# Kernel optimization log

Measured on AMD Instinct MI355X. Metric: run time of the kernel, lower is better.

Reference implementation:

```python
import jax, jax.numpy as jnp
import numpy as np

BN_EPS = 1e-5  # torch BatchNorm1d default


def setup_inputs() -> dict:
    key = jax.random.key(0)
    k = jax.random.split(key, 5)
    B, D, L = 4096, 4096, 4  # batch, width, num layers (3 hidden + 1 output)
    x = jax.random.normal(k[0], (B, D), dtype=jnp.float32)
    # Per-layer Linear weights stored as [L, in, out]; scaled like xavier-ish init.
    W = jax.random.normal(k[1], (L, D, D), dtype=jnp.float32) * (1.0 / np.sqrt(D))
    b = jax.random.normal(k[2], (L, D), dtype=jnp.float32) * 0.01
    gamma = jax.random.uniform(k[3], (L, D), dtype=jnp.float32, minval=0.5, maxval=1.5)
    beta = jax.random.normal(k[4], (L, D), dtype=jnp.float32) * 0.1
    return {"x": x, "W": W, "b": b, "gamma": gamma, "beta": beta}


def _layer(h, W_l, b_l, gamma_l, beta_l):
    # one big GEMM replaces the per-neuron GEMV loop + stack
    h = h @ W_l + b_l  # [B, out]
    # BatchNorm1d, training mode: biased batch stats over the batch dim
    mu = jnp.mean(h, axis=0)
    var = jnp.var(h, axis=0)
    h = (h - mu) * jax.lax.rsqrt(var + BN_EPS) * gamma_l + beta_l
    return jax.nn.relu(h)


def reference(x, W, b, gamma, beta):
    out = x
    for l in range(W.shape[0]):  # small fixed layer count
        out = _layer(out, W[l], b[l], gamma[l], beta[l])
    # nn.Softmax(dim=0): softmax over the batch dimension, as in the original
    return jax.nn.softmax(out, axis=0)
```

## Files before the change

### kernel.cpp

```cpp
#include <hip/hip_runtime.h>
#include <stdint.h>

#define DIMD 4096
#define DIMB 4096
#define NLAYER 4
#define NT (DIMD / 64)

typedef unsigned short u16;
typedef __attribute__((ext_vector_type(4))) float f32x4;
typedef __attribute__((ext_vector_type(8))) __bf16 bf16x8;

__device__ __forceinline__ u16 f2bf(float f) {
    union { float f; uint32_t u; } v; v.f = f;
    return (u16)((v.u + 0x7fffu + ((v.u >> 16) & 1u)) >> 16);
}
__device__ __forceinline__ float bf2f(u16 u) {
    union { uint32_t u; float f; } v; v.u = ((uint32_t)u) << 16;
    return v.f;
}

__global__ void k_cvt(const float* __restrict__ in, u16* __restrict__ out) {
    int i = (blockIdx.x * 256 + threadIdx.x) * 4;
    float4 v = *reinterpret_cast<const float4*>(in + i);
    ushort4 r;
    r.x = f2bf(v.x); r.y = f2bf(v.y); r.z = f2bf(v.z); r.w = f2bf(v.w);
    *reinterpret_cast<ushort4*>(out + i) = r;
}

__global__ void k_trans(const float* __restrict__ W, u16* __restrict__ Wt) {
    __shared__ float tile[64][65];
    const int t = threadIdx.x;
    const size_t loff = (size_t)blockIdx.z * DIMD * DIMD;
    const int n0 = blockIdx.x * 64, k0 = blockIdx.y * 64;
    const int kr = t >> 4, c4 = (t & 15) * 4;
    #pragma unroll
    for (int r = 0; r < 4; ++r) {
        float4 v = *reinterpret_cast<const float4*>(W + loff + (size_t)(k0 + kr + r * 16) * DIMD + n0 + c4);
        tile[kr + r * 16][c4 + 0] = v.x;
        tile[kr + r * 16][c4 + 1] = v.y;
        tile[kr + r * 16][c4 + 2] = v.z;
        tile[kr + r * 16][c4 + 3] = v.w;
    }
    __syncthreads();
    const int nr = t >> 4, k4 = (t & 15) * 4;
    #pragma unroll
    for (int r = 0; r < 4; ++r) {
        int n = nr + r * 16;
        ushort4 o;
        o.x = f2bf(tile[k4 + 0][n]);
        o.y = f2bf(tile[k4 + 1][n]);
        o.z = f2bf(tile[k4 + 2][n]);
        o.w = f2bf(tile[k4 + 3][n]);
        *reinterpret_cast<ushort4*>(Wt + loff + (size_t)(n0 + n) * DIMD + k0 + k4) = o;
    }
}

#define GLD(g, l) __builtin_amdgcn_global_load_lds( \
    (__attribute__((address_space(1))) void*)(g),   \
    (__attribute__((address_space(3))) void*)(l), 16, 0, 0)

__global__ __launch_bounds__(512, 2) void k_gemm(
        const u16* __restrict__ A, const u16* __restrict__ Bt,
        const float* __restrict__ bias, u16* __restrict__ H,
        float* __restrict__ csum, float* __restrict__ csum2) {
    __shared__ __attribute__((aligned(16))) u16 As[2 * 256 * 64];
    __shared__ __attribute__((aligned(16))) u16 Bs[2 * 256 * 64];
    const int tid = threadIdx.x;
    const int lane = tid & 63, wv = tid >> 6;
    const int wm = wv >> 2, wn = wv & 3;
    const int bid = blockIdx.y * 16 + blockIdx.x;
    const int swz = (bid & 7) * 32 + (bid >> 3);
    const int bm = swz >> 4, bn = swz & 15;
    const int lr = lane & 15, lk = lane >> 4;

    const int r0 = tid >> 3;
    const int cswz = (tid & 7) ^ (r0 & 7);
    const u16* gA = A  + (size_t)(bm * 256 + r0) * DIMD + cswz * 8;
    const u16* gB = Bt + (size_t)(bn * 256 + r0) * DIMD + cswz * 8;

#define STAGE_A(h, t, buf) do { \
    const u16* _s = gA + (size_t)(h) * 128 * DIMD + (size_t)(t) * 64; \
    u16* _d = As + (buf) * 16384 + (h) * 8192 + wv * 512; \
    GLD(_s, _d); GLD(_s + (size_t)64 * DIMD, _d + 4096); \
} while (0)
#define STAGE_B(h, t, buf) do { \
    const u16* _s = gB + (size_t)(h) * 128 * DIMD + (size_t)(t) * 64; \
    u16* _d = Bs + (buf) * 16384 + (h) * 8192 + wv * 512; \
    GLD(_s, _d); GLD(_s + (size_t)64 * DIMD, _d + 4096); \
} while (0)

    int aoff[4][2], boff[2][2];
    #pragma unroll
    for (int mf = 0; mf < 4; ++mf)
        #pragma unroll
        for (int ks = 0; ks < 2; ++ks) {
            int row = wm * 128 + mf * 16 + lr;
            aoff[mf][ks] = row * 64 + ((ks * 4 + lk) ^ (row & 7)) * 8;
        }
    #pragma unroll
    for (int nf = 0; nf < 2; ++nf)
        #pragma unroll
        for (int ks = 0; ks < 2; ++ks) {
            int row = wn * 64 + nf * 16 + lr;
            boff[nf][ks] = row * 64 + ((ks * 4 + lk) ^ (row & 7)) * 8;
        }

    f32x4 acc[8][4] = {};
    bf16x8 a[4][2], b0[2][2], b1[2][2];

    STAGE_B(0, 0, 0); STAGE_B(1, 0, 0); STAGE_A(0, 0, 0); STAGE_A(1, 0, 0);
    STAGE_B(0, 1, 1); STAGE_B(1, 1, 1); STAGE_A(0, 1, 1); STAGE_A(1, 1, 1);
    asm volatile("s_waitcnt vmcnt(8)" ::: "memory");
    __builtin_amdgcn_s_barrier();

    for (int t = 0; t < NT; ++t) {
        const int cur = t & 1;
        const u16* Ab = As + cur * 16384;
        const u16* Bb = Bs + cur * 16384;
        const bool pf = (t + 2 < NT);

        #pragma unroll
        for (int mf = 0; mf < 4; ++mf)
            #pragma unroll
            for (int ks = 0; ks < 2; ++ks)
                a[mf][ks] = *reinterpret_cast<const bf16x8*>(Ab + aoff[mf][ks]);
        #pragma unroll
        for (int nf = 0; nf < 2; ++nf)
            #pragma unroll
            for (int ks = 0; ks < 2; ++ks)
                b0[nf][ks] = *reinterpret_cast<const bf16x8*>(Bb + boff[nf][ks]);
        __builtin_amdgcn_s_barrier();
        asm volatile("s_waitcnt lgkmcnt(0)" ::: "memory");
        __builtin_amdgcn_s_setprio(1);
        #pragma unroll
        for (int mf = 0; mf < 4; ++mf)
            #pragma unroll
            for (int nf = 0; nf < 2; ++nf)
                #pragma unroll
                for (int ks = 0; ks < 2; ++ks)
                    acc[mf][nf] = __builtin_amdgcn_mfma_f32_16x16x32_bf16(
                        a[mf][ks], b0[nf][ks], acc[mf][nf], 0, 0, 0);
        __builtin_amdgcn_s_setprio(0);
        __builtin_amdgcn_s_barrier();

        #pragma unroll
        for (int nf = 0; nf < 2; ++nf)
            #pragma unroll
            for (int ks = 0; ks < 2; ++ks)
                b1[nf][ks] = *reinterpret_cast<const bf16x8*>(Bb + 2048 + boff[nf][ks]);
        __builtin_amdgcn_s_barrier();
        asm volatile("s_waitcnt lgkmcnt(0)" ::: "memory");
        __builtin_amdgcn_s_setprio(1);
        #pragma unroll
        for (int mf = 0; mf < 4; ++mf)
            #pragma unroll
            for (int nf = 0; nf < 2; ++nf)
                #pragma unroll
                for (int ks = 0; ks < 2; ++ks)
                    acc[mf][2 + nf] = __builtin_amdgcn_mfma_f32_16x16x32_bf16(
                        a[mf][ks], b1[nf][ks], acc[mf][2 + nf], 0, 0, 0);
        __builtin_amdgcn_s_setprio(0);
        __builtin_amdgcn_s_barrier();

        #pragma unroll
        for (int mf = 0; mf < 4; ++mf)
            #pragma unroll
            for (int ks = 0; ks < 2; ++ks)
                a[mf][ks] = *reinterpret_cast<const bf16x8*>(Ab + 4096 + aoff[mf][ks]);
        if (pf) { STAGE_B(0, t + 2, cur); STAGE_B(1, t + 2, cur); }
        __builtin_amdgcn_s_barrier();
        asm volatile("s_waitcnt lgkmcnt(0)" ::: "memory");
        __builtin_amdgcn_s_setprio(1);
        #pragma unroll
        for (int mf = 0; mf < 4; ++mf)
            #pragma unroll
            for (int nf = 0; nf < 2; ++nf)
                #pragma unroll
                for (int ks = 0; ks < 2; ++ks)
                    acc[4 + mf][2 + nf] = __builtin_amdgcn_mfma_f32_16x16x32_bf16(
                        a[mf][ks], b1[nf][ks], acc[4 + mf][2 + nf], 0, 0, 0);
        __builtin_amdgcn_s_setprio(0);
        __builtin_amdgcn_s_barrier();

        if (pf) { STAGE_A(0, t + 2, cur); STAGE_A(1, t + 2, cur); }
        __builtin_amdgcn_s_setprio(1);
        #pragma unroll
        for (int mf = 0; mf < 4; ++mf)
            #pragma unroll
            for (int nf = 0; nf < 2; ++nf)
                #pragma unroll
                for (int ks = 0; ks < 2; ++ks)
                    acc[4 + mf][nf] = __builtin_amdgcn_mfma_f32_16x16x32_bf16(
                        a[mf][ks], b0[nf][ks], acc[4 + mf][nf], 0, 0, 0);
        __builtin_amdgcn_s_setprio(0);
        if (pf) asm volatile("s_waitcnt vmcnt(8)" ::: "memory");
        else    asm volatile("s_waitcnt vmcnt(0)" ::: "memory");
        __builtin_amdgcn_s_barrier();
    }

    #pragma unroll
    for (int nh = 0; nh < 2; ++nh)
        #pragma unroll
        for (int nf = 0; nf < 2; ++nf) {
            int n = nh * 2 + nf;
            int col = bn * 256 + wn * 64 + nh * 32 + nf * 16 + lr;
            float bv = bias[col];
            float s1 = 0.f, s2 = 0.f;
            #pragma unroll
            for (int m = 0; m < 8; ++m) {
                int rbase = bm * 256 + wm * 128 + (m >> 2) * 64 + (m & 3) * 16 + lk * 4;
                #pragma unroll
                for (int r = 0; r < 4; ++r) {
                    float v = acc[m][n][r] + bv;
                    H[(size_t)(rbase + r) * DIMD + col] = f2bf(v);
                    s1 += v; s2 += v * v;
                }
            }
            s1 += __shfl_xor(s1, 16); s1 += __shfl_xor(s1, 32);
            s2 += __shfl_xor(s2, 16); s2 += __shfl_xor(s2, 32);
            if (lk == 0) {
                atomicAdd(&csum[col], s1);
                atomicAdd(&csum2[col], s2);
            }
        }
#undef STAGE_A
#undef STAGE_B
}

__global__ void k_norm(const u16* __restrict__ H, const float* __restrict__ sum,
                       const float* __restrict__ sum2, const float* __restrict__ gamma,
                       const float* __restrict__ beta, u16* __restrict__ o) {
    int j = (blockIdx.x * 256 + threadIdx.x) * 4;
    int i0 = blockIdx.y * 32;
    float4 sm = *reinterpret_cast<const float4*>(sum + j);
    float4 s2 = *reinterpret_cast<const float4*>(sum2 + j);
    float4 gm = *reinterpret_cast<const float4*>(gamma + j);
    float4 bt = *reinterpret_cast<const float4*>(beta + j);
    float s[4], tt[4];
    #pragma unroll
    for (int c = 0; c < 4; ++c) {
        float mu = (&sm.x)[c] * (1.0f / DIMB);
        float var = (&s2.x)[c] * (1.0f / DIMB) - mu * mu;
        s[c] = (&gm.x)[c] * rsqrtf(var + 1e-5f);
        tt[c] = (&bt.x)[c] - mu * s[c];
    }
    for (int i = i0; i < i0 + 32; ++i) {
        ushort4 h = *reinterpret_cast<const ushort4*>(H + (size_t)i * DIMD + j);
        ushort4 r;
        #pragma unroll
        for (int c = 0; c < 4; ++c)
            (&r.x)[c] = f2bf(fmaxf(bf2f((&h.x)[c]) * s[c] + tt[c], 0.0f));
        *reinterpret_cast<ushort4*>(o + (size_t)i * DIMD + j) = r;
    }
}

__global__ void k_esum(const u16* __restrict__ H, const float* __restrict__ sum,
                       const float* __restrict__ sum2, const float* __restrict__ gamma,
                       const float* __restrict__ beta, float* __restrict__ esum) {
    int j = (blockIdx.x * 256 + threadIdx.x) * 4;
    int i0 = blockIdx.y * 32;
    float4 sm = *reinterpret_cast<const float4*>(sum + j);
    float4 s2 = *reinterpret_cast<const float4*>(sum2 + j);
    float4 gm = *reinterpret_cast<const float4*>(gamma + j);
    float4 bt = *reinterpret_cast<const float4*>(beta + j);
    float s[4], tt[4], acc[4] = {0.f, 0.f, 0.f, 0.f};
    #pragma unroll
    for (int c = 0; c < 4; ++c) {
        float mu = (&sm.x)[c] * (1.0f / DIMB);
        float var = (&s2.x)[c] * (1.0f / DIMB) - mu * mu;
        s[c] = (&gm.x)[c] * rsqrtf(var + 1e-5f);
        tt[c] = (&bt.x)[c] - mu * s[c];
    }
    for (int i = i0; i < i0 + 32; ++i) {
        ushort4 h = *reinterpret_cast<const ushort4*>(H + (size_t)i * DIMD + j);
        #pragma unroll
        for (int c = 0; c < 4; ++c)
            acc[c] += __expf(fmaxf(bf2f((&h.x)[c]) * s[c] + tt[c], 0.0f));
    }
    #pragma unroll
    for (int c = 0; c < 4; ++c) atomicAdd(&esum[j + c], acc[c]);
}

__global__ void k_final(const u16* __restrict__ H, const float* __restrict__ sum,
                        const float* __restrict__ sum2, const float* __restrict__ gamma,
                        const float* __restrict__ beta, const float* __restrict__ esum,
                        float* __restrict__ out) {
    int j = (blockIdx.x * 256 + threadIdx.x) * 4;
    int i0 = blockIdx.y * 32;
    float4 sm = *reinterpret_cast<const float4*>(sum + j);
    float4 s2 = *reinterpret_cast<const float4*>(sum2 + j);
    float4 gm = *reinterpret_cast<const float4*>(gamma + j);
    float4 bt = *reinterpret_cast<const float4*>(beta + j);
    float4 es = *reinterpret_cast<const float4*>(esum + j);
    float s[4], tt[4], inv[4];
    #pragma unroll
    for (int c = 0; c < 4; ++c) {
        float mu = (&sm.x)[c] * (1.0f / DIMB);
        float var = (&s2.x)[c] * (1.0f / DIMB) - mu * mu;
        s[c] = (&gm.x)[c] * rsqrtf(var + 1e-5f);
        tt[c] = (&bt.x)[c] - mu * s[c];
        inv[c] = 1.0f / (&es.x)[c];
    }
    for (int i = i0; i < i0 + 32; ++i) {
        ushort4 h = *reinterpret_cast<const ushort4*>(H + (size_t)i * DIMD + j);
        float4 o;
        #pragma unroll
        for (int c = 0; c < 4; ++c)
            (&o.x)[c] = __expf(fmaxf(bf2f((&h.x)[c]) * s[c] + tt[c], 0.0f)) * inv[c];
        *reinterpret_cast<float4*>(out + (size_t)i * DIMD + j) = o;
    }
}

extern "C" void kernel_launch(void* const* d_in, const int* in_sizes, int n_in,
                              void* d_out, int out_size, void* d_ws, size_t ws_size,
                              hipStream_t stream) {
    (void)in_sizes; (void)n_in; (void)out_size; (void)ws_size;
    const float* x     = (const float*)d_in[0];
    const float* W     = (const float*)d_in[1];
    const float* b     = (const float*)d_in[2];
    const float* gamma = (const float*)d_in[3];
    const float* beta  = (const float*)d_in[4];
    float* out = (float*)d_out;

    char* ws = (char*)d_ws;
    u16*  Abf = (u16*)ws;
    u16*  Wt4 = (u16*)(ws + (size_t)32 * 1024 * 1024);
    u16*  Hbf = (u16*)(ws + (size_t)160 * 1024 * 1024);
    float* stats = (float*)(ws + (size_t)192 * 1024 * 1024);
    hipMemsetAsync(stats, 0, (4 * 8192 + 4096) * sizeof(float), stream);

    k_cvt<<<DIMB * DIMD / 1024, 256, 0, stream>>>(x, Abf);
    k_trans<<<dim3(64, 64, 4), 256, 0, stream>>>(W, Wt4);

    for (int l = 0; l < NLAYER; ++l) {
        float* sum = stats + l * 8192;
        float* sum2 = sum + 4096;
        k_gemm<<<dim3(16, 16), 512, 0, stream>>>(Abf, Wt4 + (size_t)l * DIMD * DIMD,
                                                 b + l * DIMD, Hbf, sum, sum2);
        if (l < NLAYER - 1)
            k_norm<<<dim3(4, 128), 256, 0, stream>>>(Hbf, sum, sum2,
                gamma + l * DIMD, beta + l * DIMD, Abf);
        else
            k_esum<<<dim3(4, 128), 256, 0, stream>>>(Hbf, sum, sum2,
                gamma + l * DIMD, beta + l * DIMD, stats + 32768);
    }
    k_final<<<dim3(4, 128), 256, 0, stream>>>(Hbf, stats + 3 * 8192, stats + 3 * 8192 + 4096,
        gamma + 3 * DIMD, beta + 3 * DIMD, stats + 32768, out);
}
```

Baseline: 731.1 us.

## Restructure GEMM main loop into k-step phases and write final layer fp32 into output

Reorders the GEMM inner loop so each phase loads one k-slice of A and B fragments (4x4 MFMA per phase), replaces the A-tile double prefetch with a one-ahead A stage and two-ahead B stage, and uses partial lgkmcnt waits with sched_barriers. It also drops the block-index swizzle in favour of a plain grid mapping. The last layer's GEMM writes fp32 pre-activations directly into the output buffer, and the softmax kernels read and overwrite it in place, removing the bf16 rounding of the final layer. The plain mapping may lower L2 reuse, and the fp32 store doubles write traffic for that layer.

```diff
diff --git a/kernel.cpp b/kernel.cpp
--- a/kernel.cpp
+++ b/kernel.cpp
@@ -62,15 +62,14 @@
 __global__ __launch_bounds__(512, 2) void k_gemm(
         const u16* __restrict__ A, const u16* __restrict__ Bt,
         const float* __restrict__ bias, u16* __restrict__ H,
+        float* __restrict__ Hf,
         float* __restrict__ csum, float* __restrict__ csum2) {
     __shared__ __attribute__((aligned(16))) u16 As[2 * 256 * 64];
     __shared__ __attribute__((aligned(16))) u16 Bs[2 * 256 * 64];
     const int tid = threadIdx.x;
     const int lane = tid & 63, wv = tid >> 6;
     const int wm = wv >> 2, wn = wv & 3;
-    const int bid = blockIdx.y * 16 + blockIdx.x;
-    const int swz = (bid & 7) * 32 + (bid >> 3);
-    const int bm = swz >> 4, bn = swz & 15;
+    const int bm = blockIdx.y, bn = blockIdx.x;
     const int lr = lane & 15, lk = lane >> 4;
 
     const int r0 = tid >> 3;
@@ -89,7 +88,7 @@
     GLD(_s, _d); GLD(_s + (size_t)64 * DIMD, _d + 4096); \
 } while (0)
 
-    int aoff[4][2], boff[2][2];
+    int aoff[4][2], boff[4][2];
     #pragma unroll
     for (int mf = 0; mf < 4; ++mf)
         #pragma unroll
@@ -98,7 +97,7 @@
             aoff[mf][ks] = row * 64 + ((ks * 4 + lk) ^ (row & 7)) * 8;
         }
     #pragma unroll
-    for (int nf = 0; nf < 2; ++nf)
+    for (int nf = 0; nf < 4; ++nf)
         #pragma unroll
         for (int ks = 0; ks < 2; ++ks) {
             int row = wn * 64 + nf * 16 + lr;
@@ -106,123 +105,113 @@
         }
 
     f32x4 acc[8][4] = {};
-    bf16x8 a[4][2], b0[2][2], b1[2][2];
-
-    STAGE_B(0, 0, 0); STAGE_B(1, 0, 0); STAGE_A(0, 0, 0); STAGE_A(1, 0, 0);
-    STAGE_B(0, 1, 1); STAGE_B(1, 1, 1); STAGE_A(0, 1, 1); STAGE_A(1, 1, 1);
-    asm volatile("s_waitcnt vmcnt(8)" ::: "memory");
+    bf16x8 aS0[4], aS1[4], bk0[4], bk1[4];
+
+    STAGE_B(0, 0, 0); STAGE_B(1, 0, 0);
+    STAGE_B(0, 1, 1); STAGE_B(1, 1, 1);
+    STAGE_A(0, 0, 0); STAGE_A(1, 0, 0);
+    asm volatile("s_waitcnt vmcnt(0)" ::: "memory");
     __builtin_amdgcn_s_barrier();
 
     for (int t = 0; t < NT; ++t) {
         const int cur = t & 1;
         const u16* Ab = As + cur * 16384;
         const u16* Bb = Bs + cur * 16384;
-        const bool pf = (t + 2 < NT);
-
-        #pragma unroll
-        for (int mf = 0; mf < 4; ++mf)
-            #pragma unroll
-            for (int ks = 0; ks < 2; ++ks)
-                a[mf][ks] = *reinterpret_cast<const bf16x8*>(Ab + aoff[mf][ks]);
-        #pragma unroll
-        for (int nf = 0; nf < 2; ++nf)
-            #pragma unroll
-            for (int ks = 0; ks < 2; ++ks)
-                b0[nf][ks] = *reinterpret_cast<const bf16x8*>(Bb + boff[nf][ks]);
-        __builtin_amdgcn_s_barrier();
-        asm volatile("s_waitcnt lgkmcnt(0)" ::: "memory");
+
+        if (t + 1 < NT) { STAGE_A(0, t + 1, cur ^ 1); STAGE_A(1, t + 1, cur ^ 1); }
+        #pragma unroll
+        for (int mf = 0; mf < 4; ++mf)
+            aS0[mf] = *reinterpret_cast<const bf16x8*>(Ab + aoff[mf][0]);
+        #pragma unroll
+        for (int nf = 0; nf < 4; ++nf)
+            bk0[nf] = *reinterpret_cast<const bf16x8*>(Bb + boff[nf][0]);
+        #pragma unroll
+        for (int mf = 0; mf < 4; ++mf)
+            aS1[mf] = *reinterpret_cast<const bf16x8*>(Ab + 4096 + aoff[mf][0]);
+        asm volatile("s_waitcnt lgkmcnt(4)" ::: "memory");
+        __builtin_amdgcn_sched_barrier(0);
         __builtin_amdgcn_s_setprio(1);
         #pragma unroll
         for (int mf = 0; mf < 4; ++mf)
             #pragma unroll
-            for (int nf = 0; nf < 2; ++nf)
-                #pragma unroll
-                for (int ks = 0; ks < 2; ++ks)
-                    acc[mf][nf] = __builtin_amdgcn_mfma_f32_16x16x32_bf16(
-                        a[mf][ks], b0[nf][ks], acc[mf][nf], 0, 0, 0);
+            for (int nf = 0; nf < 4; ++nf)
+                acc[mf][nf] = __builtin_amdgcn_mfma_f32_16x16x32_bf16(
+                    aS0[mf], bk0[nf], acc[mf][nf], 0, 0, 0);
         __builtin_amdgcn_s_setprio(0);
         __builtin_amdgcn_s_barrier();
 
         #pragma unroll
-        for (int nf = 0; nf < 2; ++nf)
-            #pragma unroll
-            for (int ks = 0; ks < 2; ++ks)
-                b1[nf][ks] = *reinterpret_cast<const bf16x8*>(Bb + 2048 + boff[nf][ks]);
-        __builtin_amdgcn_s_barrier();
-        asm volatile("s_waitcnt lgkmcnt(0)" ::: "memory");
+        for (int mf = 0; mf < 4; ++mf)
+            aS0[mf] = *reinterpret_cast<const bf16x8*>(Ab + 4096 + aoff[mf][1]);
+        #pragma unroll
+        for (int nf = 0; nf < 4; ++nf)
+            bk1[nf] = *reinterpret_cast<const bf16x8*>(Bb + boff[nf][1]);
+        asm volatile("s_waitcnt lgkmcnt(8)" ::: "memory");
+        __builtin_amdgcn_sched_barrier(0);
         __builtin_amdgcn_s_setprio(1);
         #pragma unroll
         for (int mf = 0; mf < 4; ++mf)
             #pragma unroll
-            for (int nf = 0; nf < 2; ++nf)
-                #pragma unroll
-                for (int ks = 0; ks < 2; ++ks)
-                    acc[mf][2 + nf] = __builtin_amdgcn_mfma_f32_16x16x32_bf16(
-                        a[mf][ks], b1[nf][ks], acc[mf][2 + nf], 0, 0, 0);
+            for (int nf = 0; nf < 4; ++nf)
+                acc[4 + mf][nf] = __builtin_amdgcn_mfma_f32_16x16x32_bf16(
+                    aS1[mf], bk0[nf], acc[4 + mf][nf], 0, 0, 0);
         __builtin_amdgcn_s_setprio(0);
         __builtin_amdgcn_s_barrier();
 
         #pragma unroll
         for (int mf = 0; mf < 4; ++mf)
-            #pragma unroll
-            for (int ks = 0; ks < 2; ++ks)
-                a[mf][ks] = *reinterpret_cast<const bf16x8*>(Ab + 4096 + aoff[mf][ks]);
-        if (pf) { STAGE_B(0, t + 2, cur); STAGE_B(1, t + 2, cur); }
-        __builtin_amdgcn_s_barrier();
-        asm volatile("s_waitcnt lgkmcnt(0)" ::: "memory");
+            aS1[mf] = *reinterpret_cast<const bf16x8*>(Ab + aoff[mf][1]);
+        asm volatile("s_waitcnt lgkmcnt(4)" ::: "memory");
+        __builtin_amdgcn_sched_barrier(0);
         __builtin_amdgcn_s_setprio(1);
         #pragma unroll
         for (int mf = 0; mf < 4; ++mf)
             #pragma unroll
-            for (int nf = 0; nf < 2; ++nf)
-                #pragma unroll
-                for (int ks = 0; ks < 2; ++ks)
-                    acc[4 + mf][2 + nf] = __builtin_amdgcn_mfma_f32_16x16x32_bf16(
-                        a[mf][ks], b1[nf][ks], acc[4 + mf][2 + nf], 0, 0, 0);
+            for (int nf = 0; nf < 4; ++nf)
+                acc[4 + mf][nf] = __builtin_amdgcn_mfma_f32_16x16x32_bf16(
+                    aS0[mf], bk1[nf], acc[4 + mf][nf], 0, 0, 0);
         __builtin_amdgcn_s_setprio(0);
         __builtin_amdgcn_s_barrier();
 
-        if (pf) { STAGE_A(0, t + 2, cur); STAGE_A(1, t + 2, cur); }
+        if (t + 2 < NT) { STAGE_B(0, t + 2, cur); STAGE_B(1, t + 2, cur); }
+        asm volatile("s_waitcnt lgkmcnt(0)" ::: "memory");
+        __builtin_amdgcn_sched_barrier(0);
         __builtin_amdgcn_s_setprio(1);
         #pragma unroll
         for (int mf = 0; mf < 4; ++mf)
             #pragma unroll
-            for (int nf = 0; nf < 2; ++nf)
-                #pragma unroll
-                for (int ks = 0; ks < 2; ++ks)
-                    acc[4 + mf][nf] = __builtin_amdgcn_mfma_f32_16x16x32_bf16(
-                        a[mf][ks], b0[nf][ks], acc[4 + mf][nf], 0, 0, 0);
+            for (int nf = 0; nf < 4; ++nf)
+                acc[mf][nf] = __builtin_amdgcn_mfma_f32_16x16x32_bf16(
+                    aS1[mf], bk1[nf], acc[mf][nf], 0, 0, 0);
         __builtin_amdgcn_s_setprio(0);
-        if (pf) asm volatile("s_waitcnt vmcnt(8)" ::: "memory");
-        else    asm volatile("s_waitcnt vmcnt(0)" ::: "memory");
+        if (t + 2 < NT) asm volatile("s_waitcnt vmcnt(4)" ::: "memory");
+        else            asm volatile("s_waitcnt vmcnt(0)" ::: "memory");
         __builtin_amdgcn_s_barrier();
     }
 
     #pragma unroll
-    for (int nh = 0; nh < 2; ++nh)
-        #pragma unroll
-        for (int nf = 0; nf < 2; ++nf) {
-            int n = nh * 2 + nf;
-            int col = bn * 256 + wn * 64 + nh * 32 + nf * 16 + lr;
-            float bv = bias[col];
-            float s1 = 0.f, s2 = 0.f;
-            #pragma unroll
-            for (int m = 0; m < 8; ++m) {
-                int rbase = bm * 256 + wm * 128 + (m >> 2) * 64 + (m & 3) * 16 + lk * 4;
-                #pragma unroll
-                for (int r = 0; r < 4; ++r) {
-                    float v = acc[m][n][r] + bv;
-                    H[(size_t)(rbase + r) * DIMD + col] = f2bf(v);
-                    s1 += v; s2 += v * v;
-                }
-            }
-            s1 += __shfl_xor(s1, 16); s1 += __shfl_xor(s1, 32);
-            s2 += __shfl_xor(s2, 16); s2 += __shfl_xor(s2, 32);
-            if (lk == 0) {
-                atomicAdd(&csum[col], s1);
-                atomicAdd(&csum2[col], s2);
+    for (int nf = 0; nf < 4; ++nf) {
+        int col = bn * 256 + wn * 64 + nf * 16 + lr;
+        float bv = bias[col];
+        float s1 = 0.f, s2 = 0.f;
+        #pragma unroll
+        for (int m = 0; m < 8; ++m) {
+            int rbase = bm * 256 + wm * 128 + (m >> 2) * 64 + (m & 3) * 16 + lk * 4;
+            #pragma unroll
+            for (int r = 0; r < 4; ++r) {
+                float v = acc[m][nf][r] + bv;
+                if (Hf) Hf[(size_t)(rbase + r) * DIMD + col] = v;
+                else    H [(size_t)(rbase + r) * DIMD + col] = f2bf(v);
+                s1 += v; s2 += v * v;
             }
         }
+        s1 += __shfl_xor(s1, 16); s1 += __shfl_xor(s1, 32);
+        s2 += __shfl_xor(s2, 16); s2 += __shfl_xor(s2, 32);
+        if (lk == 0) {
+            atomicAdd(&csum[col], s1);
+            atomicAdd(&csum2[col], s2);
+        }
+    }
 #undef STAGE_A
 #undef STAGE_B
 }
@@ -254,7 +243,7 @@
     }
 }
 
-__global__ void k_esum(const u16* __restrict__ H, const float* __restrict__ sum,
+__global__ void k_esum(const float* __restrict__ H, const float* __restrict__ sum,
                        const float* __restrict__ sum2, const float* __restrict__ gamma,
                        const float* __restrict__ beta, float* __restrict__ esum) {
     int j = (blockIdx.x * 256 + threadIdx.x) * 4;
@@ -272,19 +261,18 @@
         tt[c] = (&bt.x)[c] - mu * s[c];
     }
     for (int i = i0; i < i0 + 32; ++i) {
-        ushort4 h = *reinterpret_cast<const ushort4*>(H + (size_t)i * DIMD + j);
+        float4 h = *reinterpret_cast<const float4*>(H + (size_t)i * DIMD + j);
         #pragma unroll
         for (int c = 0; c < 4; ++c)
-            acc[c] += __expf(fmaxf(bf2f((&h.x)[c]) * s[c] + tt[c], 0.0f));
+            acc[c] += __expf(fmaxf((&h.x)[c] * s[c] + tt[c], 0.0f));
     }
     #pragma unroll
     for (int c = 0; c < 4; ++c) atomicAdd(&esum[j + c], acc[c]);
 }
 
-__global__ void k_final(const u16* __restrict__ H, const float* __restrict__ sum,
+__global__ void k_final(float* __restrict__ H, const float* __restrict__ sum,
                         const float* __restrict__ sum2, const float* __restrict__ gamma,
-                        const float* __restrict__ beta, const float* __restrict__ esum,
-                        float* __restrict__ out) {
+                        const float* __restrict__ beta, const float* __restrict__ esum) {
     int j = (blockIdx.x * 256 + threadIdx.x) * 4;
     int i0 = blockIdx.y * 32;
     float4 sm = *reinterpret_cast<const float4*>(sum + j);
@@ -302,12 +290,12 @@
         inv[c] = 1.0f / (&es.x)[c];
     }
     for (int i = i0; i < i0 + 32; ++i) {
-        ushort4 h = *reinterpret_cast<const ushort4*>(H + (size_t)i * DIMD + j);
+        float4 h = *reinterpret_cast<const float4*>(H + (size_t)i * DIMD + j);
         float4 o;
         #pragma unroll
         for (int c = 0; c < 4; ++c)
-            (&o.x)[c] = __expf(fmaxf(bf2f((&h.x)[c]) * s[c] + tt[c], 0.0f)) * inv[c];
-        *reinterpret_cast<float4*>(out + (size_t)i * DIMD + j) = o;
+            (&o.x)[c] = __expf(fmaxf((&h.x)[c] * s[c] + tt[c], 0.0f)) * inv[c];
+        *reinterpret_cast<float4*>(H + (size_t)i * DIMD + j) = o;
     }
 }
 
@@ -335,15 +323,15 @@
     for (int l = 0; l < NLAYER; ++l) {
         float* sum = stats + l * 8192;
         float* sum2 = sum + 4096;
+        float* Hf = (l == NLAYER - 1) ? out : nullptr;
         k_gemm<<<dim3(16, 16), 512, 0, stream>>>(Abf, Wt4 + (size_t)l * DIMD * DIMD,
-                                                 b + l * DIMD, Hbf, sum, sum2);
+                                                 b + l * DIMD, Hbf, Hf, sum, sum2);
         if (l < NLAYER - 1)
             k_norm<<<dim3(4, 128), 256, 0, stream>>>(Hbf, sum, sum2,
                 gamma + l * DIMD, beta + l * DIMD, Abf);
-        else
-            k_esum<<<dim3(4, 128), 256, 0, stream>>>(Hbf, sum, sum2,
-                gamma + l * DIMD, beta + l * DIMD, stats + 32768);
-    }
-    k_final<<<dim3(4, 128), 256, 0, stream>>>(Hbf, stats + 3 * 8192, stats + 3 * 8192 + 4096,
-        gamma + 3 * DIMD, beta + 3 * DIMD, stats + 32768, out);
-}
+    }
+    k_esum<<<dim3(4, 128), 256, 0, stream>>>(out, stats + 3 * 8192, stats + 3 * 8192 + 4096,
+        gamma + 3 * DIMD, beta + 3 * DIMD, stats + 32768);
+    k_final<<<dim3(4, 128), 256, 0, stream>>>(out, stats + 3 * 8192, stats + 3 * 8192 + 4096,
+        gamma + 3 * DIMD, beta + 3 * DIMD, stats + 32768);
+}
```

New measurement: 785.7 us. 7.5% more time.
